# Performance work log

Measured on AMD Instinct MI355X. Metric: run time of the kernel, lower is better.

The kernel has to match this reference:

```python
import jax, jax.numpy as jnp
import numpy as np
from jax import lax

B, T, D, H = 2, 1024, 1024, 16
DH = D // H          # 64; n_features=0 -> feature_dim = d_head
FF = 4 * D           # 4096
EPS = 1e-6           # module eps
LN_EPS = 1e-5        # torch LayerNorm default


def phi(x):
    # feature_map(kind='elu'): elu(x) + 1 (standard linear-attention feature map)
    return jax.nn.elu(x) + 1.0


def layer_norm(x, g, b):
    m = jnp.mean(x, axis=-1, keepdims=True)
    v = jnp.mean((x - m) ** 2, axis=-1, keepdims=True)
    return (x - m) / jnp.sqrt(v + LN_EPS) * g + b


def setup_inputs() -> dict:
    key = jax.random.key(0)
    ks = jax.random.split(key, 8)
    s = 0.02
    return {
        "x": jax.random.normal(ks[0], (B, T, D), jnp.float32),
        "attention_mask": jnp.ones((B, T), jnp.int32),
        "Wq": jax.random.normal(ks[1], (D, D), jnp.float32) * s,
        "Wk": jax.random.normal(ks[2], (D, D), jnp.float32) * s,
        "Wv": jax.random.normal(ks[3], (D, D), jnp.float32) * s,
        "Wo": jax.random.normal(ks[4], (D, D), jnp.float32) * s,
        "ln_attn_g": jnp.ones((D,), jnp.float32),
        "ln_attn_b": jnp.zeros((D,), jnp.float32),
        "ln_mlp_g": jnp.ones((D,), jnp.float32),
        "ln_mlp_b": jnp.zeros((D,), jnp.float32),
        "W1": jax.random.normal(ks[5], (D, FF), jnp.float32) * s,
        "b1": jnp.zeros((FF,), jnp.float32),
        "W2": jax.random.normal(ks[6], (FF, D), jnp.float32) * s,
        "b2": jnp.zeros((D,), jnp.float32),
    }


def reference(x, attention_mask, Wq, Wk, Wv, Wo, ln_attn_g, ln_attn_b,
              ln_mlp_g, ln_mlp_b, W1, b1, W2, b2):
    bsz, seq_len, _ = x.shape
    residual = x
    h = layer_norm(x, ln_attn_g, ln_attn_b)
    q = (h @ Wq).reshape(bsz, seq_len, H, DH)
    k = (h @ Wk).reshape(bsz, seq_len, H, DH)
    v = (h @ Wv).reshape(bsz, seq_len, H, DH)
    qf = phi(q)
    kf = phi(k)
    mask = attention_mask.astype(x.dtype)[:, :, None, None]  # [b,t,1,1]
    kf = kf * mask
    v = v * mask

    # causal linear attention: cumsum over t of k⊗v, expressed as lax.scan
    qs = jnp.moveaxis(qf, 1, 0)  # [t,b,h,f]
    ks = jnp.moveaxis(kf, 1, 0)
    vs = jnp.moveaxis(v, 1, 0)

    S0 = jnp.zeros((bsz, H, DH, DH), x.dtype)  # running sum of k⊗v
    z0 = jnp.zeros((bsz, H, DH), x.dtype)      # running sum of k

    def step(carry, qkv):
        S, z = carry
        q_t, k_t, v_t = qkv
        S = S + jnp.einsum('bhf,bhd->bhfd', k_t, v_t)
        z = z + k_t
        num = jnp.einsum('bhf,bhfd->bhd', q_t, S)
        den = jnp.einsum('bhf,bhf->bh', q_t, z)
        return (S, z), num / (den[..., None] + EPS)

    _, outs = lax.scan(step, (S0, z0), (qs, ks, vs))  # [t,b,h,d]
    attn_out = jnp.moveaxis(outs, 0, 1).reshape(bsz, seq_len, D)

    x = residual + attn_out @ Wo  # dropout in eval mode = identity
    residual = x
    h = layer_norm(x, ln_mlp_g, ln_mlp_b)
    mlp = jax.nn.gelu(h @ W1 + b1, approximate=False) @ W2 + b2
    return residual + mlp
```

## Files before the change

kernel.cpp:

```cpp
#include <hip/hip_runtime.h>
#include <math.h>


typedef __attribute__((ext_vector_type(8))) __bf16 bf16x8;
typedef __attribute__((ext_vector_type(8))) unsigned short us8;
typedef __attribute__((ext_vector_type(4))) float f32x4;

__device__ __forceinline__ unsigned short f2bf(float f) {
  unsigned int u = __builtin_bit_cast(unsigned int, f);
  unsigned int r = (u + 0x7fffu + ((u >> 16) & 1u)) >> 16;
  return (unsigned short)r;
}
__device__ __forceinline__ float bf2f(unsigned short u) {
  return __builtin_bit_cast(float, ((unsigned int)u) << 16);
}
__device__ __forceinline__ float phi_fn(float x) {
  return x > 0.f ? x + 1.f : __expf(x);
}

__device__ __forceinline__ void gload16(const unsigned short* g, unsigned short* l) {
  __builtin_amdgcn_global_load_lds(
      (const __attribute__((address_space(1))) unsigned int*)(const void*)g,
      (__attribute__((address_space(3))) unsigned int*)(void*)l, 16, 0, 0);
}

__device__ __forceinline__ void cvt_tile(
    const float* __restrict__ W, unsigned short* __restrict__ WT,
    int K, int N, int tk, int tn, int tid)
{
  __shared__ unsigned short tile[64][72];
  const int n0 = tn * 64, k0 = tk * 64;
  for (int it = 0; it < 16; ++it) {
    const int lin = it * 256 + tid;
    const int i = lin >> 6, j = lin & 63;
    tile[j][i] = f2bf(W[(size_t)(k0 + i) * N + n0 + j]);
  }
  __syncthreads();
  for (int it = 0; it < 16; ++it) {
    const int lin = it * 256 + tid;
    const int j = lin >> 6, i = lin & 63;
    WT[(size_t)(n0 + j) * K + k0 + i] = tile[j][i];
  }
}

__global__ __launch_bounds__(256) void cvt_all(
    const float* __restrict__ Wq, const float* __restrict__ Wk,
    const float* __restrict__ Wv, const float* __restrict__ Wo,
    const float* __restrict__ W1, const float* __restrict__ W2,
    unsigned short* __restrict__ WqkvT, unsigned short* __restrict__ WoT,
    unsigned short* __restrict__ W1T, unsigned short* __restrict__ W2T)
{
  const int bid = blockIdx.x, tid = threadIdx.x;
  if (bid < 768) {
    const int wsel = bid >> 8, local = bid & 255;
    const float* W = wsel == 0 ? Wq : (wsel == 1 ? Wk : Wv);
    cvt_tile(W, WqkvT + (size_t)wsel * 1024 * 1024, 1024, 1024, local >> 4, local & 15, tid);
  } else if (bid < 1024) {
    const int local = bid - 768;
    cvt_tile(Wo, WoT, 1024, 1024, local >> 4, local & 15, tid);
  } else if (bid < 2048) {
    const int local = bid - 1024;
    cvt_tile(W1, W1T, 1024, 4096, local >> 6, local & 63, tid);
  } else {
    const int local = bid - 2048;
    cvt_tile(W2, W2T, 4096, 1024, local >> 4, local & 15, tid);
  }
}

__global__ __launch_bounds__(256) void ln_to_bf16(
    const float* __restrict__ x, const float* __restrict__ g,
    const float* __restrict__ b, unsigned short* __restrict__ out)
{
  const int row = blockIdx.x;
  const int tid = threadIdx.x;
  const float4 xv = *(const float4*)&x[(size_t)row * 1024 + tid * 4];
  float xa[4] = {xv.x, xv.y, xv.z, xv.w};
  float s = xa[0] + xa[1] + xa[2] + xa[3];
  float sq = xa[0]*xa[0] + xa[1]*xa[1] + xa[2]*xa[2] + xa[3]*xa[3];
  for (int off = 32; off > 0; off >>= 1) {
    s += __shfl_down(s, off);
    sq += __shfl_down(sq, off);
  }
  __shared__ float red[8];
  if ((tid & 63) == 0) { red[tid >> 6] = s; red[4 + (tid >> 6)] = sq; }
  __syncthreads();
  const float ts = red[0] + red[1] + red[2] + red[3];
  const float tq = red[4] + red[5] + red[6] + red[7];
  const float mean = ts * (1.f / 1024.f);
  const float var = tq * (1.f / 1024.f) - mean * mean;
  const float inv = rsqrtf(var + 1e-5f);
  unsigned short o[4];
#pragma unroll
  for (int j = 0; j < 4; ++j) {
    const int col = tid * 4 + j;
    o[j] = f2bf((xa[j] - mean) * inv * g[col] + b[col]);
  }
  unsigned int p0 = (unsigned)o[0] | ((unsigned)o[1] << 16);
  unsigned int p1 = (unsigned)o[2] | ((unsigned)o[3] << 16);
  *(uint2*)(out + (size_t)row * 1024 + tid * 4) = make_uint2(p0, p1);
}

enum { EPI_QKV = 0, EPI_WO = 1, EPI_W1 = 2, EPI_PART = 3 };

template <int BM, int BN, int EPI>
__global__ __launch_bounds__(256) void gemm_bf16(
    const unsigned short* __restrict__ A,
    const unsigned short* __restrict__ BT,
    const float* __restrict__ bias, const float* __restrict__ res,
    const int* __restrict__ mask,
    float* __restrict__ outF, unsigned short* __restrict__ outB,
    int M, int N, int K, int lda, int ldb)
{
  constexpr int FM = BM / 32, FN = BN / 32;
  constexpr int IA = BM / 32, IB = BN / 32;
  __shared__ __align__(16) unsigned short lA[2][BM * 64];
  __shared__ __align__(16) unsigned short lB[2][BN * 64];
  const int tid = threadIdx.x;

  int bn_i, bm_i;
  {
    const int gx = gridDim.x, gy = gridDim.y;
    const int i = blockIdx.x + blockIdx.y * gx;
    const int nwg = gx * gy;
    if (((nwg & 63) == 0) && ((gx & 3) == 0) && ((gy & 1) == 0)) {
      const int k8 = i & 7, j = i >> 3;
      const int G = k8 + (j >> 3) * 8;
      const int p = j & 7;
      const int sgx = gx >> 2;
      bm_i = (G / sgx) * 2 + (p >> 2);
      bn_i = (G % sgx) * 4 + (p & 3);
    } else { bn_i = blockIdx.x; bm_i = blockIdx.y; }
  }
  const int bn0 = bn_i * BN, bm0 = bm_i * BM;
  const int kz = blockIdx.z;
  A  += (size_t)kz * K;
  BT += (size_t)kz * K;
  if constexpr (EPI == EPI_PART) outF += (size_t)kz * M * N;

  const int w = tid >> 6, l = tid & 63;
  const int wm = (w >> 1) * (BM / 2), wn = (w & 1) * (BN / 2);
  const int r16 = l & 15, g = l >> 4;
  const int srow8 = l >> 3;
  const int scolg = ((l & 7) ^ srow8) * 8;
  f32x4 acc[FM][FN] = {};

  const unsigned short* Ab = A + (size_t)bm0 * lda;
  const unsigned short* Bb = BT + (size_t)bn0 * ldb;
  const int nsteps = K >> 6;

  auto stage = [&](int s, int buf) {
    const int kc = s << 6;
#pragma unroll
    for (int ii = 0; ii < IA; ++ii) {
      const int r0 = (w * IA + ii) * 8;
      gload16(&Ab[(size_t)(r0 + srow8) * lda + kc + scolg], &lA[buf][r0 * 64]);
    }
#pragma unroll
    for (int ii = 0; ii < IB; ++ii) {
      const int r0 = (w * IB + ii) * 8;
      gload16(&Bb[(size_t)(r0 + srow8) * ldb + kc + scolg], &lB[buf][r0 * 64]);
    }
  };

  stage(0, 0);
  int cur = 0;
  for (int s = 0; s < nsteps; ++s) {
    __syncthreads();
    if (s + 1 < nsteps) stage(s + 1, cur ^ 1);
#pragma unroll
    for (int h = 0; h < 2; ++h) {
      bf16x8 av[FM], bv[FN];
#pragma unroll
      for (int mi = 0; mi < FM; ++mi) {
        const int row = wm + mi * 16 + r16;
        const int grp = (h * 4 + g) ^ (r16 & 7);
        av[mi] = __builtin_bit_cast(bf16x8, *(const us8*)&lA[cur][row * 64 + grp * 8]);
      }
#pragma unroll
      for (int ni = 0; ni < FN; ++ni) {
        const int row = wn + ni * 16 + r16;
        const int grp = (h * 4 + g) ^ (r16 & 7);
        bv[ni] = __builtin_bit_cast(bf16x8, *(const us8*)&lB[cur][row * 64 + grp * 8]);
      }
#pragma unroll
      for (int mi = 0; mi < FM; ++mi)
#pragma unroll
        for (int ni = 0; ni < FN; ++ni)
          acc[mi][ni] = __builtin_amdgcn_mfma_f32_16x16x32_bf16(av[mi], bv[ni], acc[mi][ni], 0, 0, 0);
    }
    cur ^= 1;
  }

#pragma unroll
  for (int mi = 0; mi < FM; ++mi) {
#pragma unroll
    for (int r = 0; r < 4; ++r) {
      const int grow = bm0 + wm + mi * 16 + g * 4 + r;
      float mrow = 0.f;
      if constexpr (EPI == EPI_QKV) mrow = (float)mask[grow];
#pragma unroll
      for (int ni = 0; ni < FN; ++ni) {
        const int gcol = bn0 + wn + ni * 16 + r16;
        const size_t o = (size_t)grow * N + gcol;
        const float v = acc[mi][ni][r];
        if constexpr (EPI == EPI_QKV) {
          const int seg = (bn0 + wn + ni * 16) >> 10;
          const float rv = (seg == 0) ? phi_fn(v) : (seg == 1 ? phi_fn(v) * mrow : v * mrow);
          outB[o] = f2bf(rv);
        } else if constexpr (EPI == EPI_WO) {
          outF[o] = v + res[o];
        } else if constexpr (EPI == EPI_W1) {
          const float t = v + bias[gcol];
          outB[o] = f2bf(0.5f * t * (1.f + erff(t * 0.70710678118654752f)));
        } else if constexpr (EPI == EPI_PART) {
          outF[o] = v;
        }
      }
    }
  }
}

__global__ __launch_bounds__(256) void reduce_w2(
    const float* __restrict__ part, const float* __restrict__ res,
    const float* __restrict__ bias, float* __restrict__ out)
{
  const int row = blockIdx.x, tid = threadIdx.x;
  const size_t o = (size_t)row * 1024 + tid * 4;
  const float4 p0 = *(const float4*)&part[o];
  const float4 p1 = *(const float4*)&part[(size_t)2048 * 1024 + o];
  const float4 r = *(const float4*)&res[o];
  const float4 b = *(const float4*)&bias[tid * 4];
  float4 s;
  s.x = p0.x + p1.x + r.x + b.x;
  s.y = p0.y + p1.y + r.y + b.y;
  s.z = p0.z + p1.z + r.z + b.z;
  s.w = p0.w + p1.w + r.w + b.w;
  *(float4*)&out[o] = s;
}

__global__ __launch_bounds__(256) void chunk_sums(
    const unsigned short* __restrict__ qkvB, float* __restrict__ S,
    float* __restrict__ z)
{
  __shared__ float kS[64][68];
  __shared__ float vS[64][68];
  const int blk = blockIdx.x;
  const int bh = blk >> 4, c = blk & 15;
  const int b = bh >> 4, h = bh & 15;
  const int tid = threadIdx.x;
  const size_t base = ((size_t)(b * 1024 + c * 64)) * 3072 + h * 64;
  for (int it = 0; it < 2; ++it) {
    const int lin = it * 256 + tid;
    const int t = lin >> 3, f8 = (lin & 7) * 8;
    const us8 k8 = *(const us8*)&qkvB[base + 1024 + (size_t)t * 3072 + f8];
    const us8 v8 = *(const us8*)&qkvB[base + 2048 + (size_t)t * 3072 + f8];
#pragma unroll
    for (int j = 0; j < 8; ++j) {
      kS[t][f8 + j] = bf2f(k8[j]);
      vS[t][f8 + j] = bf2f(v8[j]);
    }
  }
  __syncthreads();
  const int fq = tid >> 2, dg = (tid & 3) * 16;
  float acc[16] = {};
  for (int t = 0; t < 64; ++t) {
    const float kk = kS[t][fq];
#pragma unroll
    for (int j = 0; j < 4; ++j) {
      const float4 vv = *(const float4*)&vS[t][dg + j * 4];
      acc[j*4+0] += kk * vv.x; acc[j*4+1] += kk * vv.y;
      acc[j*4+2] += kk * vv.z; acc[j*4+3] += kk * vv.w;
    }
  }
  float* Sp = S + ((size_t)bh * 16 + c) * 4096;
#pragma unroll
  for (int i = 0; i < 16; ++i) Sp[(size_t)fq * 64 + dg + i] = acc[i];
  if (tid < 64) {
    float s = 0.f;
    for (int t = 0; t < 64; ++t) s += kS[t][tid];
    z[((size_t)bh * 16 + c) * 64 + tid] = s;
  }
}

__global__ __launch_bounds__(256) void scan_chunks(
    float* __restrict__ S, float* __restrict__ z)
{
  const int bh = blockIdx.x >> 3, sub = blockIdx.x & 7;
  const int tid = threadIdx.x;
  float* base = S + (size_t)bh * 16 * 4096 + sub * 512 + tid * 2;
  float r0 = 0.f, r1 = 0.f;
  for (int c = 0; c < 16; ++c) {
    float2* p = (float2*)(base + (size_t)c * 4096);
    const float2 cur = *p;
    *p = make_float2(r0, r1);
    r0 += cur.x; r1 += cur.y;
  }
  if (sub == 0 && tid < 64) {
    float zr = 0.f;
    for (int c = 0; c < 16; ++c) {
      float* zp = z + ((size_t)bh * 16 + c) * 64 + tid;
      const float cur = *zp; *zp = zr; zr += cur;
    }
  }
}

__global__ __launch_bounds__(256) void attn_out_kernel(
    const unsigned short* __restrict__ qkvB, const float* __restrict__ Sp,
    const float* __restrict__ zp, unsigned short* __restrict__ attnB)
{
  __shared__ float qS[64][68];
  __shared__ float kvS[64][68];
  __shared__ float pS[64][68];
  __shared__ float zS[64];
  __shared__ float den[64];
  const int blk = blockIdx.x;
  const int bh = blk >> 4, c = blk & 15;
  const int b = bh >> 4, h = bh & 15;
  const int tid = threadIdx.x;
  const size_t base = ((size_t)(b * 1024 + c * 64)) * 3072 + h * 64;
  const size_t obase = ((size_t)(b * 1024 + c * 64)) * 1024 + h * 64;

  for (int it = 0; it < 2; ++it) {
    const int lin = it * 256 + tid;
    const int t = lin >> 3, f8 = (lin & 7) * 8;
    const us8 q8 = *(const us8*)&qkvB[base + (size_t)t * 3072 + f8];
    const us8 k8 = *(const us8*)&qkvB[base + 1024 + (size_t)t * 3072 + f8];
#pragma unroll
    for (int j = 0; j < 8; ++j) {
      qS[t][f8 + j] = bf2f(q8[j]);
      kvS[t][f8 + j] = bf2f(k8[j]);
    }
  }
  if (tid < 64) zS[tid] = zp[((size_t)bh * 16 + c) * 64 + tid];
  __syncthreads();

  const int tr = tid >> 4, tc = tid & 15;
  float p[4][4] = {};
  for (int f = 0; f < 64; ++f) {
    float qv[4], kv[4];
#pragma unroll
    for (int i = 0; i < 4; ++i) { qv[i] = qS[tr*4+i][f]; kv[i] = kvS[tc*4+i][f]; }
#pragma unroll
    for (int i = 0; i < 4; ++i)
#pragma unroll
      for (int j = 0; j < 4; ++j) p[i][j] += qv[i] * kv[j];
  }
#pragma unroll
  for (int i = 0; i < 4; ++i)
#pragma unroll
    for (int j = 0; j < 4; ++j) {
      const int t = tr*4 + i, t2 = tc*4 + j;
      pS[t][t2] = (t2 <= t) ? p[i][j] : 0.f;
    }
  __syncthreads();
  for (int it = 0; it < 2; ++it) {
    const int lin = it * 256 + tid;
    const int t = lin >> 3, f8 = (lin & 7) * 8;
    const us8 v8 = *(const us8*)&qkvB[base + 2048 + (size_t)t * 3072 + f8];
#pragma unroll
    for (int j = 0; j < 8; ++j) kvS[t][f8 + j] = bf2f(v8[j]);
  }
  if (tid < 64) {
    const int t = tid;
    float d = 0.f;
    for (int f = 0; f < 64; ++f) d += qS[t][f] * zS[f];
    for (int t2 = 0; t2 <= t; ++t2) d += pS[t][t2];
    den[t] = d + 1e-6f;
  }
  __syncthreads();

  const float* SpB = Sp + ((size_t)bh * 16 + c) * 4096;
  float o[4][4] = {};
  for (int f = 0; f < 64; ++f) {
    float qv[4];
#pragma unroll
    for (int i = 0; i < 4; ++i) qv[i] = qS[tr*4+i][f];
    const float4 sv = *(const float4*)&SpB[(size_t)f * 64 + tc * 4];
#pragma unroll
    for (int i = 0; i < 4; ++i) {
      o[i][0] += qv[i]*sv.x; o[i][1] += qv[i]*sv.y;
      o[i][2] += qv[i]*sv.z; o[i][3] += qv[i]*sv.w;
    }
  }
  for (int t2 = 0; t2 < 64; ++t2) {
    float pv[4];
#pragma unroll
    for (int i = 0; i < 4; ++i) pv[i] = pS[tr*4+i][t2];
    const float4 vv = *(const float4*)&kvS[t2][tc * 4];
#pragma unroll
    for (int i = 0; i < 4; ++i) {
      o[i][0] += pv[i]*vv.x; o[i][1] += pv[i]*vv.y;
      o[i][2] += pv[i]*vv.z; o[i][3] += pv[i]*vv.w;
    }
  }
#pragma unroll
  for (int i = 0; i < 4; ++i) {
    const int t = tr*4 + i;
    const float dinv = 1.f / den[t];
#pragma unroll
    for (int j = 0; j < 4; ++j)
      attnB[obase + (size_t)t * 1024 + tc * 4 + j] = f2bf(o[i][j] * dinv);
  }
}

extern "C" void kernel_launch(void* const* d_in, const int* in_sizes, int n_in,
                              void* d_out, int out_size, void* d_ws, size_t ws_size,
                              hipStream_t stream)
{
  (void)in_sizes; (void)n_in; (void)out_size; (void)ws_size;
  const float* x   = (const float*)d_in[0];
  const int*   msk = (const int*)d_in[1];
  const float* Wq  = (const float*)d_in[2];
  const float* Wk  = (const float*)d_in[3];
  const float* Wv  = (const float*)d_in[4];
  const float* Wo  = (const float*)d_in[5];
  const float* g1  = (const float*)d_in[6];
  const float* be1 = (const float*)d_in[7];
  const float* g2  = (const float*)d_in[8];
  const float* be2 = (const float*)d_in[9];
  const float* W1  = (const float*)d_in[10];
  const float* b1  = (const float*)d_in[11];
  const float* W2  = (const float*)d_in[12];
  const float* b2  = (const float*)d_in[13];
  float* out = (float*)d_out;

  char* ws = (char*)d_ws;
  const size_t MB = 1024 * 1024;
  unsigned short* WqkvT = (unsigned short*)(ws + 0 * MB);
  unsigned short* WoT   = (unsigned short*)(ws + 6 * MB);
  unsigned short* W1T   = (unsigned short*)(ws + 8 * MB);
  unsigned short* W2T   = (unsigned short*)(ws + 16 * MB);
  unsigned short* hB    = (unsigned short*)(ws + 24 * MB);
  unsigned short* qkvB  = (unsigned short*)(ws + 28 * MB);
  float* Ssum = (float*)(ws + 40 * MB);
  float* zsum = (float*)(ws + 48 * MB);
  unsigned short* attnB = (unsigned short*)(ws + 49 * MB);
  float* x2   = (float*)(ws + 53 * MB);
  unsigned short* h2B = (unsigned short*)(ws + 61 * MB);
  unsigned short* ffB = (unsigned short*)(ws + 65 * MB);
  float* part = (float*)(ws + 28 * MB);

  const dim3 B256(256);
  cvt_all<<<3072, B256, 0, stream>>>(Wq, Wk, Wv, Wo, W1, W2, WqkvT, WoT, W1T, W2T);
  ln_to_bf16<<<2048, B256, 0, stream>>>(x, g1, be1, hB);

  gemm_bf16<128, 128, EPI_QKV><<<dim3(24, 16), B256, 0, stream>>>(
      hB, WqkvT, nullptr, nullptr, msk, nullptr, qkvB, 2048, 3072, 1024, 1024, 1024);

  chunk_sums<<<512, B256, 0, stream>>>(qkvB, Ssum, zsum);
  scan_chunks<<<256, B256, 0, stream>>>(Ssum, zsum);
  attn_out_kernel<<<512, B256, 0, stream>>>(qkvB, Ssum, zsum, attnB);

  gemm_bf16<128, 64, EPI_WO><<<dim3(16, 16), B256, 0, stream>>>(
      attnB, WoT, nullptr, x, nullptr, x2, nullptr, 2048, 1024, 1024, 1024, 1024);

  ln_to_bf16<<<2048, B256, 0, stream>>>(x2, g2, be2, h2B);

  gemm_bf16<128, 128, EPI_W1><<<dim3(32, 16), B256, 0, stream>>>(
      h2B, W1T, b1, nullptr, nullptr, nullptr, ffB, 2048, 4096, 1024, 1024, 1024);

  gemm_bf16<128, 64, EPI_PART><<<dim3(16, 16, 2), B256, 0, stream>>>(
      ffB, W2T, nullptr, nullptr, nullptr, part, nullptr, 2048, 1024, 2048, 4096, 4096);
  reduce_w2<<<2048, B256, 0, stream>>>(part, x2, b2, out);
}
```

Measured before the change: 263.0 us.

## Deepen GEMM prefetch to two stages, fuse first LayerNorm into weight conversion

The bf16 GEMM main loop now keeps two K-tiles in flight. It uses explicit vmcnt waits and raw barriers, loads all LDS fragments for a step into registers before issuing the next-next stage, and raises wave priority around the MFMA block. The first LayerNorm launch is merged into the weight conversion kernel as extra blocks, which removes one kernel launch. The chunk scan kernel now batches its 16 loads before storing. The hand-written waitcnt literals tie correctness to the exact number of loads per stage, and the extra barrier per step adds sync cost.

```diff
diff --git a/kernel.cpp b/kernel.cpp
--- a/kernel.cpp
+++ b/kernel.cpp
@@ -22,6 +22,45 @@
   __builtin_amdgcn_global_load_lds(
       (const __attribute__((address_space(1))) unsigned int*)(const void*)g,
       (__attribute__((address_space(3))) unsigned int*)(void*)l, 16, 0, 0);
+}
+
+__device__ __forceinline__ void ln_row(
+    const float* __restrict__ x, const float* __restrict__ g,
+    const float* __restrict__ b, unsigned short* __restrict__ out,
+    int row, int tid)
+{
+  const float4 xv = *(const float4*)&x[(size_t)row * 1024 + tid * 4];
+  float xa[4] = {xv.x, xv.y, xv.z, xv.w};
+  float s = xa[0] + xa[1] + xa[2] + xa[3];
+  float sq = xa[0]*xa[0] + xa[1]*xa[1] + xa[2]*xa[2] + xa[3]*xa[3];
+  for (int off = 32; off > 0; off >>= 1) {
+    s += __shfl_down(s, off);
+    sq += __shfl_down(sq, off);
+  }
+  __shared__ float red[8];
+  if ((tid & 63) == 0) { red[tid >> 6] = s; red[4 + (tid >> 6)] = sq; }
+  __syncthreads();
+  const float ts = red[0] + red[1] + red[2] + red[3];
+  const float tq = red[4] + red[5] + red[6] + red[7];
+  const float mean = ts * (1.f / 1024.f);
+  const float var = tq * (1.f / 1024.f) - mean * mean;
+  const float inv = rsqrtf(var + 1e-5f);
+  unsigned short o[4];
+#pragma unroll
+  for (int j = 0; j < 4; ++j) {
+    const int col = tid * 4 + j;
+    o[j] = f2bf((xa[j] - mean) * inv * g[col] + b[col]);
+  }
+  unsigned int p0 = (unsigned)o[0] | ((unsigned)o[1] << 16);
+  unsigned int p1 = (unsigned)o[2] | ((unsigned)o[3] << 16);
+  *(uint2*)(out + (size_t)row * 1024 + tid * 4) = make_uint2(p0, p1);
+}
+
+__global__ __launch_bounds__(256) void ln_to_bf16(
+    const float* __restrict__ x, const float* __restrict__ g,
+    const float* __restrict__ b, unsigned short* __restrict__ out)
+{
+  ln_row(x, g, b, out, blockIdx.x, threadIdx.x);
 }
 
 __device__ __forceinline__ void cvt_tile(
@@ -48,7 +87,9 @@
     const float* __restrict__ Wv, const float* __restrict__ Wo,
     const float* __restrict__ W1, const float* __restrict__ W2,
     unsigned short* __restrict__ WqkvT, unsigned short* __restrict__ WoT,
-    unsigned short* __restrict__ W1T, unsigned short* __restrict__ W2T)
+    unsigned short* __restrict__ W1T, unsigned short* __restrict__ W2T,
+    const float* __restrict__ x, const float* __restrict__ g1,
+    const float* __restrict__ be1, unsigned short* __restrict__ hB)
 {
   const int bid = blockIdx.x, tid = threadIdx.x;
   if (bid < 768) {
@@ -61,43 +102,12 @@
   } else if (bid < 2048) {
     const int local = bid - 1024;
     cvt_tile(W1, W1T, 1024, 4096, local >> 6, local & 63, tid);
-  } else {
+  } else if (bid < 3072) {
     const int local = bid - 2048;
     cvt_tile(W2, W2T, 4096, 1024, local >> 4, local & 15, tid);
-  }
-}
-
-__global__ __launch_bounds__(256) void ln_to_bf16(
-    const float* __restrict__ x, const float* __restrict__ g,
-    const float* __restrict__ b, unsigned short* __restrict__ out)
-{
-  const int row = blockIdx.x;
-  const int tid = threadIdx.x;
-  const float4 xv = *(const float4*)&x[(size_t)row * 1024 + tid * 4];
-  float xa[4] = {xv.x, xv.y, xv.z, xv.w};
-  float s = xa[0] + xa[1] + xa[2] + xa[3];
-  float sq = xa[0]*xa[0] + xa[1]*xa[1] + xa[2]*xa[2] + xa[3]*xa[3];
-  for (int off = 32; off > 0; off >>= 1) {
-    s += __shfl_down(s, off);
-    sq += __shfl_down(sq, off);
-  }
-  __shared__ float red[8];
-  if ((tid & 63) == 0) { red[tid >> 6] = s; red[4 + (tid >> 6)] = sq; }
-  __syncthreads();
-  const float ts = red[0] + red[1] + red[2] + red[3];
-  const float tq = red[4] + red[5] + red[6] + red[7];
-  const float mean = ts * (1.f / 1024.f);
-  const float var = tq * (1.f / 1024.f) - mean * mean;
-  const float inv = rsqrtf(var + 1e-5f);
-  unsigned short o[4];
-#pragma unroll
-  for (int j = 0; j < 4; ++j) {
-    const int col = tid * 4 + j;
-    o[j] = f2bf((xa[j] - mean) * inv * g[col] + b[col]);
-  }
-  unsigned int p0 = (unsigned)o[0] | ((unsigned)o[1] << 16);
-  unsigned int p1 = (unsigned)o[2] | ((unsigned)o[3] << 16);
-  *(uint2*)(out + (size_t)row * 1024 + tid * 4) = make_uint2(p0, p1);
+  } else {
+    ln_row(x, g1, be1, hB, bid - 3072, tid);
+  }
 }
 
 enum { EPI_QKV = 0, EPI_WO = 1, EPI_W1 = 2, EPI_PART = 3 };
@@ -113,6 +123,8 @@
 {
   constexpr int FM = BM / 32, FN = BN / 32;
   constexpr int IA = BM / 32, IB = BN / 32;
+  constexpr int LPS = IA + IB;
+  static_assert(LPS == 8 || LPS == 6, "vmcnt literal");
   __shared__ __align__(16) unsigned short lA[2][BM * 64];
   __shared__ __align__(16) unsigned short lB[2][BN * 64];
   const int tid = threadIdx.x;
@@ -163,31 +175,47 @@
   };
 
   stage(0, 0);
+  stage(1, 1);
   int cur = 0;
   for (int s = 0; s < nsteps; ++s) {
-    __syncthreads();
-    if (s + 1 < nsteps) stage(s + 1, cur ^ 1);
+    if (s + 1 < nsteps) {
+      if constexpr (LPS == 8) asm volatile("s_waitcnt vmcnt(8)" ::: "memory");
+      else                    asm volatile("s_waitcnt vmcnt(6)" ::: "memory");
+    } else {
+      asm volatile("s_waitcnt vmcnt(0)" ::: "memory");
+    }
+    __builtin_amdgcn_s_barrier();
+
+    bf16x8 av[2][FM], bv[2][FN];
 #pragma unroll
     for (int h = 0; h < 2; ++h) {
-      bf16x8 av[FM], bv[FN];
 #pragma unroll
       for (int mi = 0; mi < FM; ++mi) {
         const int row = wm + mi * 16 + r16;
         const int grp = (h * 4 + g) ^ (r16 & 7);
-        av[mi] = __builtin_bit_cast(bf16x8, *(const us8*)&lA[cur][row * 64 + grp * 8]);
+        av[h][mi] = __builtin_bit_cast(bf16x8, *(const us8*)&lA[cur][row * 64 + grp * 8]);
       }
 #pragma unroll
       for (int ni = 0; ni < FN; ++ni) {
         const int row = wn + ni * 16 + r16;
         const int grp = (h * 4 + g) ^ (r16 & 7);
-        bv[ni] = __builtin_bit_cast(bf16x8, *(const us8*)&lB[cur][row * 64 + grp * 8]);
+        bv[h][ni] = __builtin_bit_cast(bf16x8, *(const us8*)&lB[cur][row * 64 + grp * 8]);
       }
+    }
+    asm volatile("s_waitcnt lgkmcnt(0)" ::: "memory");
+    __builtin_amdgcn_sched_barrier(0);
+    __builtin_amdgcn_s_barrier();
+    if (s + 2 < nsteps) stage(s + 2, cur);
+
+    __builtin_amdgcn_s_setprio(1);
+#pragma unroll
+    for (int h = 0; h < 2; ++h)
 #pragma unroll
       for (int mi = 0; mi < FM; ++mi)
 #pragma unroll
         for (int ni = 0; ni < FN; ++ni)
-          acc[mi][ni] = __builtin_amdgcn_mfma_f32_16x16x32_bf16(av[mi], bv[ni], acc[mi][ni], 0, 0, 0);
-    }
+          acc[mi][ni] = __builtin_amdgcn_mfma_f32_16x16x32_bf16(av[h][mi], bv[h][ni], acc[mi][ni], 0, 0, 0);
+    __builtin_amdgcn_s_setprio(0);
     cur ^= 1;
   }
 
@@ -288,19 +316,24 @@
   const int bh = blockIdx.x >> 3, sub = blockIdx.x & 7;
   const int tid = threadIdx.x;
   float* base = S + (size_t)bh * 16 * 4096 + sub * 512 + tid * 2;
+  float2 v[16];
+#pragma unroll
+  for (int c = 0; c < 16; ++c) v[c] = *(float2*)(base + (size_t)c * 4096);
   float r0 = 0.f, r1 = 0.f;
+#pragma unroll
   for (int c = 0; c < 16; ++c) {
-    float2* p = (float2*)(base + (size_t)c * 4096);
-    const float2 cur = *p;
-    *p = make_float2(r0, r1);
-    r0 += cur.x; r1 += cur.y;
+    const float2 cv = v[c];
+    *(float2*)(base + (size_t)c * 4096) = make_float2(r0, r1);
+    r0 += cv.x; r1 += cv.y;
   }
   if (sub == 0 && tid < 64) {
+    float* zp = z + (size_t)bh * 16 * 64 + tid;
+    float zv[16];
+#pragma unroll
+    for (int c = 0; c < 16; ++c) zv[c] = zp[c * 64];
     float zr = 0.f;
-    for (int c = 0; c < 16; ++c) {
-      float* zp = z + ((size_t)bh * 16 + c) * 64 + tid;
-      const float cur = *zp; *zp = zr; zr += cur;
-    }
+#pragma unroll
+    for (int c = 0; c < 16; ++c) { zp[c * 64] = zr; zr += zv[c]; }
   }
 }
 
@@ -441,8 +474,8 @@
   float* part = (float*)(ws + 28 * MB);
 
   const dim3 B256(256);
-  cvt_all<<<3072, B256, 0, stream>>>(Wq, Wk, Wv, Wo, W1, W2, WqkvT, WoT, W1T, W2T);
-  ln_to_bf16<<<2048, B256, 0, stream>>>(x, g1, be1, hB);
+  cvt_all<<<5120, B256, 0, stream>>>(Wq, Wk, Wv, Wo, W1, W2, WqkvT, WoT, W1T, W2T,
+                                     x, g1, be1, hB);
 
   gemm_bf16<128, 128, EPI_QKV><<<dim3(24, 16), B256, 0, stream>>>(
       hB, WqkvT, nullptr, nullptr, msk, nullptr, qkvB, 2048, 3072, 1024, 1024, 1024);
```

After: 242.7 us. -7.7%, faster.
